# Kernel tuning notes

Measured on AMD Instinct MI355X. Metric: run time of the kernel, lower is better.

The kernel has to match this reference:

```python
import jax, jax.numpy as jnp
import numpy as np

E, K, B = 64, 8, 32
IN_DIM, OUT_DIM = 1024, 1024


def setup_inputs() -> dict:
    key = jax.random.key(0)
    k1, k2, k3, k4, k5, k6 = jax.random.split(key, 6)
    return {
        "weight_probs": jax.random.uniform(k1, (B, K), dtype=jnp.float32),
        "bias_probs": jax.random.uniform(k2, (B, K), dtype=jnp.float32),
        "weight_indices": jax.random.randint(k3, (B, K), 0, E, dtype=jnp.int64),
        "bias_indices": jax.random.randint(k4, (B, K), 0, E, dtype=jnp.int64),
        # parameter banks: one linear layer's params per expert
        "weight_bank": jax.random.normal(k5, (E, OUT_DIM, IN_DIM), dtype=jnp.float32) * 0.02,
        "bias_bank": jax.random.normal(k6, (E, OUT_DIM), dtype=jnp.float32) * 0.02,
    }


def reference(weight_probs, bias_probs, weight_indices, bias_indices, weight_bank, bias_bank):
    # _select_parameters: gather per-(batch, top_k) expert params
    sel_w = weight_bank[weight_indices]          # [B, K, O, I]
    sel_b = bias_bank[bias_indices]              # [B, K, O]
    # _compute_mixture: probability-weighted sum over the top_k axis
    weight_mixture = jnp.einsum("bk,bkoi->boi", weight_probs, sel_w)  # [B, O, I]
    bias_mixture = jnp.einsum("bk,bko->bo", bias_probs, sel_b)        # [B, O]
    return weight_mixture, bias_mixture
```

## Files before the change

### kernel.cpp

```cpp
#include <hip/hip_runtime.h>
#include <hip/hip_bf16.h>


typedef __attribute__((ext_vector_type(8)))  short short8v;
typedef __attribute__((ext_vector_type(16))) float f32x16;

constexpr int E = 64;
constexpr int K = 8;
constexpr int B = 32;
constexpr int IN_DIM = 1024;
constexpr int OUT_DIM = 1024;

constexpr int NCOL     = OUT_DIM * IN_DIM;
constexpr int BLK      = 256;
constexpr int GRID     = 1024;
constexpr int WAVES    = GRID * 4;
constexpr int STEPS    = NCOL / 32 / WAVES;
constexpr int WM_ELEMS = B * NCOL;
constexpr int OB4      = OUT_DIM / 4;

__global__ __launch_bounds__(BLK, 4) void ParameterMixture_86835648790543_kernel(
    const float* __restrict__ wprobs,
    const float* __restrict__ bprobs,
    const int*   __restrict__ widx,
    const int*   __restrict__ bidx,
    const float* __restrict__ wbank,
    const float* __restrict__ bbank,
    float*       __restrict__ out)
{
    const int bid  = blockIdx.x;
    const int t    = threadIdx.x;
    const int wv   = t >> 6;
    const int lane = t & 63;
    const int m    = lane & 31;
    const int kh   = (lane >> 5) * 8;
    const int cl   = lane & 31;

    if (bid < 32) {
        const int tt   = bid * BLK + t;
        const int b    = tt / OB4;
        const int off4 = tt % OB4;
        const float4* __restrict__ bb4 = (const float4*)bbank;
        float4 a4 = make_float4(0.f, 0.f, 0.f, 0.f);
#pragma unroll
        for (int k = 0; k < K; ++k) {
            const float p = bprobs[b * K + k];
            const int   e = bidx[b * K + k];
            const float4 v = bb4[e * OB4 + off4];
            a4.x += p * v.x; a4.y += p * v.y;
            a4.z += p * v.z; a4.w += p * v.w;
        }
        ((float4*)(out + WM_ELEMS))[tt] = a4;
    }

    float wp[K];
    int   wi[K];
#pragma unroll
    for (int k2 = 0; k2 < K; ++k2) {
        wp[k2] = wprobs[m * K + k2];
        wi[k2] = widx[m * K + k2];
    }
    short8v aH[4], aL[4];
#pragma unroll
    for (int s = 0; s < 4; ++s) {
#pragma unroll
        for (int j = 0; j < 8; ++j) {
            const int e = s * 16 + kh + j;
            float p = 0.f;
#pragma unroll
            for (int k2 = 0; k2 < K; ++k2)
                p += (wi[k2] == e) ? wp[k2] : 0.f;
            const __hip_bfloat16 h  = __float2bfloat16(p);
            const float          hf = __bfloat162float(h);
            const __hip_bfloat16 l  = __float2bfloat16(p - hf);
            aH[s][j] = __builtin_bit_cast(short, h);
            aL[s][j] = __builtin_bit_cast(short, l);
        }
    }

    const size_t ncol    = (size_t)NCOL;
    const int    wave_id = bid * 4 + wv;

#pragma unroll 1
    for (int step = 0; step < STEPS; ++step) {
        const int col0 = wave_id * (32 * STEPS) + step * 32;
        const float* __restrict__ wcol = wbank + col0 + cl;

        float w[4][8];
#pragma unroll
        for (int s = 0; s < 4; ++s)
#pragma unroll
            for (int j = 0; j < 8; ++j)
                w[s][j] = wcol[(size_t)(s * 16 + kh + j) * ncol];

        f32x16 acc;
#pragma unroll
        for (int i = 0; i < 16; ++i) acc[i] = 0.f;

#pragma unroll
        for (int s = 0; s < 4; ++s) {
            short8v bh, bl;
#pragma unroll
            for (int j = 0; j < 8; ++j) {
                const float x = w[s][j];
                const __hip_bfloat16 h  = __float2bfloat16(x);
                const float          hf = __bfloat162float(h);
                const __hip_bfloat16 l  = __float2bfloat16(x - hf);
                bh[j] = __builtin_bit_cast(short, h);
                bl[j] = __builtin_bit_cast(short, l);
            }
            acc = __builtin_amdgcn_mfma_f32_32x32x16_bf16(aH[s], bh, acc, 0, 0, 0);
            acc = __builtin_amdgcn_mfma_f32_32x32x16_bf16(aH[s], bl, acc, 0, 0, 0);
            acc = __builtin_amdgcn_mfma_f32_32x32x16_bf16(aL[s], bh, acc, 0, 0, 0);
        }

        float* __restrict__ ob = out + (size_t)((lane >> 5) * 4) * ncol + col0 + cl;
#pragma unroll
        for (int reg = 0; reg < 16; ++reg) {
            const int row = (reg & 3) + 8 * (reg >> 2);
            __builtin_nontemporal_store(acc[reg], ob + (size_t)row * ncol);
        }
    }
}

extern "C" void kernel_launch(void* const* d_in, const int* in_sizes, int n_in,
                              void* d_out, int out_size, void* d_ws, size_t ws_size,
                              hipStream_t stream) {
    const float* wprobs = (const float*)d_in[0];
    const float* bprobs = (const float*)d_in[1];
    const int*   widx   = (const int*)d_in[2];
    const int*   bidx   = (const int*)d_in[3];
    const float* wbank  = (const float*)d_in[4];
    const float* bbank  = (const float*)d_in[5];
    float*       out    = (float*)d_out;

    ParameterMixture_86835648790543_kernel<<<GRID, BLK, 0, stream>>>(
        wprobs, bprobs, widx, bidx, wbank, bbank, out);
}
```

Baseline: 96.15 us.

## Vectorize bank loads to float4, double-buffer row groups, widen column tile

Each wave now handles 128 columns per step instead of 32. Loads are float4 per lane and go into two register buffers, so the next row-group loads are issued while MFMAs run on the current one. Output stores become float4 vector stores, now regular rather than nontemporal. The grid is halved and launch bounds are relaxed to 2 blocks, so register pressure goes up (4 accumulators plus 2x8 float4 buffers) and occupancy may drop. Spills are possible.

```diff
diff --git a/kernel.cpp b/kernel.cpp
--- a/kernel.cpp
+++ b/kernel.cpp
@@ -13,13 +13,28 @@
 
 constexpr int NCOL     = OUT_DIM * IN_DIM;
 constexpr int BLK      = 256;
-constexpr int GRID     = 1024;
+constexpr int GRID     = 512;
 constexpr int WAVES    = GRID * 4;
-constexpr int STEPS    = NCOL / 32 / WAVES;
+constexpr int CPW      = NCOL / WAVES;
+constexpr int CSTEP    = 128;
+constexpr int STEPS    = CPW / CSTEP;
+constexpr int NRG      = STEPS * 4;
 constexpr int WM_ELEMS = B * NCOL;
 constexpr int OB4      = OUT_DIM / 4;
 
-__global__ __launch_bounds__(BLK, 4) void ParameterMixture_86835648790543_kernel(
+struct HL { short h; short l; };
+
+__device__ __forceinline__ HL split_bf16(float x) {
+    const __hip_bfloat16 hb = __float2bfloat16(x);
+    const float          hf = __bfloat162float(hb);
+    const __hip_bfloat16 lb = __float2bfloat16(x - hf);
+    HL r;
+    r.h = __builtin_bit_cast(short, hb);
+    r.l = __builtin_bit_cast(short, lb);
+    return r;
+}
+
+__global__ __launch_bounds__(BLK, 2) void ParameterMixture_86835648790543_kernel(
     const float* __restrict__ wprobs,
     const float* __restrict__ bprobs,
     const int*   __restrict__ widx,
@@ -70,55 +85,73 @@
 #pragma unroll
             for (int k2 = 0; k2 < K; ++k2)
                 p += (wi[k2] == e) ? wp[k2] : 0.f;
-            const __hip_bfloat16 h  = __float2bfloat16(p);
-            const float          hf = __bfloat162float(h);
-            const __hip_bfloat16 l  = __float2bfloat16(p - hf);
-            aH[s][j] = __builtin_bit_cast(short, h);
-            aL[s][j] = __builtin_bit_cast(short, l);
+            const HL r = split_bf16(p);
+            aH[s][j] = r.h;
+            aL[s][j] = r.l;
         }
     }
 
-    const size_t ncol    = (size_t)NCOL;
-    const int    wave_id = bid * 4 + wv;
+    const size_t ncol     = (size_t)NCOL;
+    const int    wave_id  = bid * 4 + wv;
+    const int    col_base = wave_id * CPW;
+
+    auto load_rg = [&](float4 (&w)[8], int g) {
+        if (g > NRG - 1) g = NRG - 1;
+        const int c0 = col_base + (g >> 2) * CSTEP + 4 * cl;
+        const int r0 = (g & 3) * 16 + kh;
+        const float* __restrict__ base = wbank + c0;
+#pragma unroll
+        for (int j = 0; j < 8; ++j)
+            w[j] = *(const float4*)(base + (size_t)(r0 + j) * ncol);
+    };
+
+    float4 bufA[8], bufB[8];
+    load_rg(bufA, 0);
+    load_rg(bufB, 1);
 
 #pragma unroll 1
     for (int step = 0; step < STEPS; ++step) {
-        const int col0 = wave_id * (32 * STEPS) + step * 32;
-        const float* __restrict__ wcol = wbank + col0 + cl;
+        f32x16 acc[4];
+#pragma unroll
+        for (int tt2 = 0; tt2 < 4; ++tt2)
+#pragma unroll
+            for (int i = 0; i < 16; ++i) acc[tt2][i] = 0.f;
 
-        float w[4][8];
-#pragma unroll
-        for (int s = 0; s < 4; ++s)
-#pragma unroll
-            for (int j = 0; j < 8; ++j)
-                w[s][j] = wcol[(size_t)(s * 16 + kh + j) * ncol];
+        const int g0 = step * 4;
 
-        f32x16 acc;
-#pragma unroll
-        for (int i = 0; i < 16; ++i) acc[i] = 0.f;
-
-#pragma unroll
-        for (int s = 0; s < 4; ++s) {
-            short8v bh, bl;
+        auto compute_rg = [&](const float4 (&w)[8], int rg) {
+            short8v bh[4], bl[4];
 #pragma unroll
             for (int j = 0; j < 8; ++j) {
-                const float x = w[s][j];
-                const __hip_bfloat16 h  = __float2bfloat16(x);
-                const float          hf = __bfloat162float(h);
-                const __hip_bfloat16 l  = __float2bfloat16(x - hf);
-                bh[j] = __builtin_bit_cast(short, h);
-                bl[j] = __builtin_bit_cast(short, l);
+                const HL rx = split_bf16(w[j].x);
+                const HL ry = split_bf16(w[j].y);
+                const HL rz = split_bf16(w[j].z);
+                const HL rw = split_bf16(w[j].w);
+                bh[0][j] = rx.h; bl[0][j] = rx.l;
+                bh[1][j] = ry.h; bl[1][j] = ry.l;
+                bh[2][j] = rz.h; bl[2][j] = rz.l;
+                bh[3][j] = rw.h; bl[3][j] = rw.l;
             }
-            acc = __builtin_amdgcn_mfma_f32_32x32x16_bf16(aH[s], bh, acc, 0, 0, 0);
-            acc = __builtin_amdgcn_mfma_f32_32x32x16_bf16(aH[s], bl, acc, 0, 0, 0);
-            acc = __builtin_amdgcn_mfma_f32_32x32x16_bf16(aL[s], bh, acc, 0, 0, 0);
-        }
+#pragma unroll
+            for (int tt2 = 0; tt2 < 4; ++tt2) {
+                acc[tt2] = __builtin_amdgcn_mfma_f32_32x32x16_bf16(aH[rg], bh[tt2], acc[tt2], 0, 0, 0);
+                acc[tt2] = __builtin_amdgcn_mfma_f32_32x32x16_bf16(aH[rg], bl[tt2], acc[tt2], 0, 0, 0);
+                acc[tt2] = __builtin_amdgcn_mfma_f32_32x32x16_bf16(aL[rg], bh[tt2], acc[tt2], 0, 0, 0);
+            }
+        };
 
-        float* __restrict__ ob = out + (size_t)((lane >> 5) * 4) * ncol + col0 + cl;
+        compute_rg(bufA, 0);  load_rg(bufA, g0 + 2);
+        compute_rg(bufB, 1);  load_rg(bufB, g0 + 3);
+        compute_rg(bufA, 2);  load_rg(bufA, g0 + 4);
+        compute_rg(bufB, 3);  load_rg(bufB, g0 + 5);
+
+        const int c0 = col_base + step * CSTEP + 4 * cl;
+        float* __restrict__ ob = out + c0 + (size_t)((lane >> 5) * 4) * ncol;
 #pragma unroll
         for (int reg = 0; reg < 16; ++reg) {
             const int row = (reg & 3) + 8 * (reg >> 2);
-            __builtin_nontemporal_store(acc[reg], ob + (size_t)row * ncol);
+            const float4 v = make_float4(acc[0][reg], acc[1][reg], acc[2][reg], acc[3][reg]);
+            *(float4*)(ob + (size_t)row * ncol) = v;
         }
     }
 }
```

Measured after the change: 93.75 us. -2.5%, faster.
